# Optimization experiments

Hardware: AMD Instinct MI355X
Metric: run time of the kernel (lower is better)

The kernel has to match this reference:

```python
import jax, jax.numpy as jnp
import numpy as np

B, L, SIZE, BACK, H = 4, 1024, 1024, 512, 16
D = SIZE // H  # head_size = 64


def setup_inputs() -> dict:
    key = jax.random.key(0)
    ks = jax.random.split(key, 18)
    s = 0.02
    return {
        "k": jax.random.normal(ks[0], (B, L, SIZE), jnp.float32),
        "v": jax.random.normal(ks[1], (B, L, SIZE), jnp.float32),
        "q": jax.random.normal(ks[2], (B, L, SIZE), jnp.float32),
        "background": jax.random.normal(ks[3], (B, L, BACK), jnp.float32),
        # weights stored [in, out] (pre-transposed vs torch Linear)
        "Wk": jax.random.normal(ks[4], (SIZE, SIZE), jnp.float32) * s,
        "bk": jnp.zeros((SIZE,), jnp.float32),
        "Wv": jax.random.normal(ks[5], (SIZE, SIZE), jnp.float32) * s,
        "bv": jnp.zeros((SIZE,), jnp.float32),
        "Wq": jax.random.normal(ks[6], (SIZE, SIZE), jnp.float32) * s,
        "bq": jnp.zeros((SIZE,), jnp.float32),
        "Wb": jax.random.normal(ks[7], (BACK, SIZE), jnp.float32) * s,
        "bb": jnp.zeros((SIZE,), jnp.float32),
        "Wo": jax.random.normal(ks[8], (SIZE, SIZE), jnp.float32) * s,
        "bo": jnp.zeros((SIZE,), jnp.float32),
    }


def _heads(x):
    # [B, L, H*D] -> [B, H, L, D]
    b, l, _ = x.shape
    return x.reshape(b, l, H, D).transpose(0, 2, 1, 3)


def reference(k, v, q, background, Wk, bk, Wv, bv, Wq, bq, Wb, bb, Wo, bo):
    kh = _heads(k @ Wk + bk)
    vh = _heads(v @ Wv + bv)
    qh = _heads(q @ Wq + bq) / jnp.sqrt(jnp.asarray(D, k.dtype))
    gh = _heads(background @ Wb + bb)
    scores = jnp.einsum("bhqd,bhkd->bhqk", qh, kh)   # [B,H,Lq,Lk]
    gates = jax.nn.sigmoid(jnp.einsum("bhqd,bhkd->bhqk", qh, gh))
    attn = jax.nn.softmax(scores, axis=-1) * gates    # dropout = identity (eval)
    ctx = jnp.einsum("bhqk,bhkd->bhqd", attn, vh)
    ctx = ctx.transpose(0, 2, 1, 3).reshape(k.shape[0], -1, H * D)
    return ctx @ Wo + bo
```

## Files before the change

### kernel.cpp

```cpp
#include <hip/hip_runtime.h>
#include <cstddef>
#include <cstdint>

typedef __attribute__((ext_vector_type(8))) short s16x8;
typedef __attribute__((ext_vector_type(4))) short s16x4;
typedef __attribute__((ext_vector_type(4))) float f32x4;
typedef __attribute__((ext_vector_type(4))) unsigned u32x4;

#define MFMA(a, b, c) __builtin_amdgcn_mfma_f32_16x16x32_bf16(a, b, c, 0, 0, 0)
#define LOG2E 1.44269504088896f

__device__ __forceinline__ short f2bf(float x) {
    uint32_t u = __float_as_uint(x);
    u = (u + 0x7FFFu + ((u >> 16) & 1u)) >> 16;
    return (short)u;
}

__device__ __forceinline__ void gld16(const void* g, void* l) {
    __builtin_amdgcn_global_load_lds(
        (const __attribute__((address_space(1))) unsigned int*)g,
        (__attribute__((address_space(3))) unsigned int*)l, 16, 0, 0);
}

__device__ __forceinline__ float fexp2(float x) {
#if __has_builtin(__builtin_amdgcn_exp2f)
    return __builtin_amdgcn_exp2f(x);
#else
    return exp2f(x);
#endif
}

__device__ __forceinline__ float frcp(float x) {
#if __has_builtin(__builtin_amdgcn_rcpf)
    return __builtin_amdgcn_rcpf(x);
#else
    return 1.f / x;
#endif
}

__device__ __forceinline__ unsigned cvtpk(float lo, float hi) {
    unsigned r;
    asm("v_cvt_pk_bf16_f32 %0, %1, %2" : "=v"(r) : "v"(lo), "v"(hi));
    return r;
}

struct WtP { const float* W[5]; short* Wt[5]; int K[5]; };

__global__ __launch_bounds__(256)
void conv_wt_b(WtP p) {
    __shared__ float T[64][65];
    const int z = blockIdx.z;
    const int K = p.K[z];
    const int k0 = blockIdx.y << 6, n0 = blockIdx.x << 6;
    if (k0 >= K) return;
    const float* W = p.W[z];
    short* Wt = p.Wt[z];
    const int tr = threadIdx.x >> 4, tc4 = (threadIdx.x & 15) << 2;
    #pragma unroll
    for (int i = 0; i < 4; ++i) {
        const int r = tr + i * 16;
        const float4 v = *(const float4*)(W + (size_t)(k0 + r) * 1024 + n0 + tc4);
        T[r][tc4 + 0] = v.x; T[r][tc4 + 1] = v.y;
        T[r][tc4 + 2] = v.z; T[r][tc4 + 3] = v.w;
    }
    __syncthreads();
    #pragma unroll
    for (int i = 0; i < 4; ++i) {
        const int nr = tr + i * 16;
        s16x4 o;
        o[0] = f2bf(T[tc4 + 0][nr]); o[1] = f2bf(T[tc4 + 1][nr]);
        o[2] = f2bf(T[tc4 + 2][nr]); o[3] = f2bf(T[tc4 + 3][nr]);
        *(s16x4*)(Wt + (size_t)(n0 + nr) * K + k0 + tc4) = o;
    }
}

struct Proj5P {
    const float* Af[5];
    const short* A[5];
    const short* Bt[5]; const float* bias[5];
    void* Y[5]; int Kd[5]; float alpha[5]; int mode[5];
};

template <int F32A>
__global__ __launch_bounds__(256, 2)
void proj_gemm128d(Proj5P p, int zbase) {
    __shared__ __align__(16) short lds[2 * 16384];

    const int tid = threadIdx.x;
    const int w = tid >> 6, lane = tid & 63;
    const int la = lane & 15, kg = lane >> 4;
    const int wr = w >> 1, wc = w & 1;

    const int cpx = gridDim.x >> 3;
    const int orig = blockIdx.x;
    const int swz = (orig & 7) * cpx + (orig >> 3);
    const int z = zbase + (swz >> 8);
    const int rem = swz & 255;
    const int bm = rem >> 3, bn = rem & 7;

    const int K = p.Kd[z];
    const int NT = K >> 6;

    const int srow = tid >> 3;
    const int csrc = (tid & 7) ^ (srow & 7);
    const float* gAf = p.Af[z] ? p.Af[z] + (size_t)(bm * 128 + srow) * K + csrc * 8 : nullptr;
    const short* gA  = p.A[z]  ? p.A[z]  + (size_t)(bm * 128 + srow) * K + csrc * 8 : nullptr;
    const short* gB  = p.Bt[z] + (size_t)(bn * 128 + srow) * K + csrc * 8;
    short* dstA = &lds[srow * 64 + (tid & 7) * 8];
    short* dstB = dstA + 8192;

    float4 av[4][2];

#define STAGE_ISSUE(t, nb) do {                                            \
        const size_t ko_ = (size_t)((t) << 6);                             \
        short* bb_ = dstB + (nb) * 16384;                                  \
        _Pragma("unroll")                                                  \
        for (int i = 0; i < 4; ++i) {                                      \
            if (F32A) {                                                    \
                av[i][0] = *(const float4*)(gAf + (size_t)(32 * i) * K + ko_);     \
                av[i][1] = *(const float4*)(gAf + (size_t)(32 * i) * K + ko_ + 4); \
            } else {                                                       \
                gld16(gA + (size_t)(32 * i) * K + ko_,                     \
                      dstA + (nb) * 16384 + i * 2048);                     \
            }                                                              \
            gld16(gB + (size_t)(32 * i) * K + ko_, bb_ + i * 2048);        \
        }                                                                  \
    } while (0)

#define A_WRITE(nb) do {                                                   \
        if (F32A) {                                                        \
            _Pragma("unroll")                                              \
            for (int i = 0; i < 4; ++i) {                                  \
                u32x4 pk;                                                  \
                pk[0] = cvtpk(av[i][0].x, av[i][0].y);                     \
                pk[1] = cvtpk(av[i][0].z, av[i][0].w);                     \
                pk[2] = cvtpk(av[i][1].x, av[i][1].y);                     \
                pk[3] = cvtpk(av[i][1].z, av[i][1].w);                     \
                *(u32x4*)(dstA + (nb) * 16384 + i * 2048) = pk;            \
            }                                                              \
        }                                                                  \
    } while (0)

    const int c0 = kg ^ (la & 7), c1 = (4 + kg) ^ (la & 7);
    const int aRd = (wr * 64 + la) * 64;
    const int bRd = 8192 + (wc * 64 + la) * 64;

    f32x4 acc[4][4] = {};

    STAGE_ISSUE(0, 0);
    asm volatile("s_waitcnt vmcnt(0)" ::: "memory");
    A_WRITE(0);
    asm volatile("s_waitcnt lgkmcnt(0)" ::: "memory");
    asm volatile("s_barrier" ::: "memory");

    for (int t = 0; t < NT; ++t) {
        const int cb = (t & 1) * 16384;
        const int nb = (t & 1) ^ 1;
        if (t + 1 < NT) STAGE_ISSUE(t + 1, nb);
        s16x8 af[4][2], bf[4][2];
        #pragma unroll
        for (int m = 0; m < 4; ++m) {
            af[m][0] = *(const s16x8*)&lds[cb + aRd + m * 1024 + c0 * 8];
            af[m][1] = *(const s16x8*)&lds[cb + aRd + m * 1024 + c1 * 8];
        }
        #pragma unroll
        for (int n = 0; n < 4; ++n) {
            bf[n][0] = *(const s16x8*)&lds[cb + bRd + n * 1024 + c0 * 8];
            bf[n][1] = *(const s16x8*)&lds[cb + bRd + n * 1024 + c1 * 8];
        }
        __builtin_amdgcn_s_setprio(1);
        #pragma unroll
        for (int m = 0; m < 4; ++m)
            #pragma unroll
            for (int n = 0; n < 4; ++n) {
                acc[m][n] = MFMA(af[m][0], bf[n][0], acc[m][n]);
                acc[m][n] = MFMA(af[m][1], bf[n][1], acc[m][n]);
            }
        __builtin_amdgcn_s_setprio(0);
        if (t + 1 < NT) {
            asm volatile("s_waitcnt vmcnt(0)" ::: "memory");
            A_WRITE(nb);
            asm volatile("s_waitcnt lgkmcnt(0)" ::: "memory");
            asm volatile("s_barrier" ::: "memory");
        }
    }
#undef STAGE_ISSUE
#undef A_WRITE

    const float* __restrict__ bias = p.bias[z];
    const float alpha = p.alpha[z];
    const int mode = p.mode[z];

    if (mode == 2) {
        short* __restrict__ Y = (short*)p.Y[z];
        short* Tv = lds;
        asm volatile("s_waitcnt lgkmcnt(0)" ::: "memory");
        asm volatile("s_barrier" ::: "memory");
        #pragma unroll
        for (int ni = 0; ni < 4; ++ni) {
            const int rrow = wc * 64 + ni * 16 + la;
            const float bs = bias[bn * 128 + rrow];
            #pragma unroll
            for (int mi = 0; mi < 4; ++mi) {
                const int l0 = wr * 64 + mi * 16 + kg * 4;
                const unsigned d0 = cvtpk(alpha * (acc[mi][ni][0] + bs),
                                          alpha * (acc[mi][ni][1] + bs));
                const unsigned d1 = cvtpk(alpha * (acc[mi][ni][2] + bs),
                                          alpha * (acc[mi][ni][3] + bs));
                *(unsigned*)&Tv[rrow * 132 + l0]     = d0;
                *(unsigned*)&Tv[rrow * 132 + l0 + 2] = d1;
            }
        }
        asm volatile("s_waitcnt lgkmcnt(0)" ::: "memory");
        asm volatile("s_barrier" ::: "memory");
        const int bb_ = (bm * 128) >> 10;
        const int l0g = (bm * 128) & 1023;
        #pragma unroll
        for (int s = 0; s < 8; ++s) {
            const int c = tid + (s << 8);
            const int rr = c >> 4, seg = c & 15;
            const int hh = bn * 2 + (rr >> 6), dd = rr & 63;
            const s16x8 vv = *(const s16x8*)&Tv[rr * 132 + seg * 8];
            *(s16x8*)&Y[((((size_t)bb_ * 16 + hh) * 64 + dd) << 10) + l0g + seg * 8] = vv;
        }
        return;
    }

    #pragma unroll
    for (int n = 0; n < 4; ++n) {
        const int col = bn * 128 + wc * 64 + n * 16 + la;
        const float bs = bias[col];
        #pragma unroll
        for (int m = 0; m < 4; ++m) {
            const int row0 = bm * 128 + wr * 64 + m * 16 + kg * 4;
            #pragma unroll
            for (int r = 0; r < 4; ++r) {
                const float v = alpha * (acc[m][n][r] + bs);
                if (mode == 0) {
                    ((short*)p.Y[z])[(size_t)(row0 + r) * 1024 + col] = f2bf(v);
                } else {
                    ((float*)p.Y[z])[(size_t)(row0 + r) * 1024 + col] = v;
                }
            }
        }
    }
}

__global__ __launch_bounds__(512)
void attn_mfma(const short* __restrict__ qh, const short* __restrict__ kh,
               const short* __restrict__ gh, const short* __restrict__ vt,
               short* __restrict__ ctx) {
    __shared__ __align__(16) short lds[33792];

    const int tid = threadIdx.x, w = tid >> 6, lane = tid & 63;
    const int la = lane & 15, kg = lane >> 4;

    const int orig = blockIdx.x;
    const int xcd = orig & 7, i = orig >> 3;
    const int bh = xcd * 8 + (i >> 3);
    const int qt = i & 7;
    const int b = bh >> 4, h = bh & 15;
    const int q0 = qt << 7;

    const size_t hb = ((size_t)b << 20) + ((size_t)h << 6);
    const size_t vtbase = ((size_t)bh) << 16;

    const int qrow = q0 + w * 16 + la;
    const s16x8 aq0 = *(const s16x8*)(qh + hb + (size_t)qrow * 1024 + kg * 8);
    const s16x8 aq1 = *(const s16x8*)(qh + hb + (size_t)qrow * 1024 + 32 + kg * 8);

    const int sr = tid >> 3, sc = tid & 7;
    const int cs = sc ^ (sr & 7);
    const short* ksrc = kh + hb + (size_t)sr * 1024 + cs * 8;
    const short* gsrc = gh + hb + (size_t)sr * 1024 + cs * 8;
    const short* vsrc = vt + vtbase + (size_t)sr * 1024 + cs * 8;
    const int sdst = tid * 8;

    const int ch0 = (kg ^ (la & 7)) * 8;
    const int ch1 = ((4 + kg) ^ (la & 7)) * 8;
    const int pbase = 24576 + w * 1152;

    float s_run = 0.f;
    f32x4 o[4] = {};

#define ASTG(kt, bb) do {                                                  \
        const size_t kr_ = (size_t)((kt) << 6) * 1024;                     \
        gld16(ksrc + kr_, &lds[(bb) * 4096 + sdst]);                       \
        gld16(gsrc + kr_, &lds[8192 + (bb) * 4096 + sdst]);                \
        gld16(vsrc + ((kt) << 6), &lds[16384 + (bb) * 4096 + sdst]);       \
    } while (0)

    ASTG(0, 0);
    asm volatile("s_waitcnt vmcnt(0)" ::: "memory");
    asm volatile("s_barrier" ::: "memory");

    for (int kt = 0; kt < 16; ++kt) {
        const int cb = (kt & 1) * 4096;
        if (kt < 15) ASTG(kt + 1, (kt + 1) & 1);

        f32x4 st[4] = {}, gt[4] = {};
        #pragma unroll
        for (int nf = 0; nf < 4; ++nf) {
            const int rb = cb + (nf * 16 + la) * 64;
            const s16x8 kb0 = *(const s16x8*)&lds[rb + ch0];
            const s16x8 kb1 = *(const s16x8*)&lds[rb + ch1];
            st[nf] = MFMA(kb0, aq0, st[nf]);
            st[nf] = MFMA(kb1, aq1, st[nf]);
            const s16x8 gb0 = *(const s16x8*)&lds[8192 + rb + ch0];
            const s16x8 gb1 = *(const s16x8*)&lds[8192 + rb + ch1];
            gt[nf] = MFMA(gb0, aq0, gt[nf]);
            gt[nf] = MFMA(gb1, aq1, gt[nf]);
        }

        float ps = 0.f;
        unsigned pkw[4][2];
        #pragma unroll
        for (int nf = 0; nf < 4; ++nf) {
            const float p0 = fexp2(st[nf][0]);
            const float p1 = fexp2(st[nf][1]);
            const float p2 = fexp2(st[nf][2]);
            const float p3 = fexp2(st[nf][3]);
            ps += (p0 + p1) + (p2 + p3);
            const float g0 = frcp(1.f + fexp2(-gt[nf][0]));
            const float g1 = frcp(1.f + fexp2(-gt[nf][1]));
            const float g2 = frcp(1.f + fexp2(-gt[nf][2]));
            const float g3 = frcp(1.f + fexp2(-gt[nf][3]));
            pkw[nf][0] = cvtpk(p0 * g0, p1 * g1);
            pkw[nf][1] = cvtpk(p2 * g2, p3 * g3);
        }
        s_run += ps;

        #pragma unroll
        for (int nf = 0; nf < 4; ++nf) {
            *(unsigned*)&lds[pbase + la * 72 + nf * 16 + kg * 4]     = pkw[nf][0];
            *(unsigned*)&lds[pbase + la * 72 + nf * 16 + kg * 4 + 2] = pkw[nf][1];
        }

        const s16x8 pa0 = *(const s16x8*)&lds[pbase + la * 72 + kg * 8];
        const s16x8 pa1 = *(const s16x8*)&lds[pbase + la * 72 + 32 + kg * 8];
        #pragma unroll
        for (int nf = 0; nf < 4; ++nf) {
            const int rb = cb + (nf * 16 + la) * 64;
            const s16x8 vb0 = *(const s16x8*)&lds[16384 + rb + ch0];
            const s16x8 vb1 = *(const s16x8*)&lds[16384 + rb + ch1];
            o[nf] = MFMA(vb0, pa0, o[nf]);
            o[nf] = MFMA(vb1, pa1, o[nf]);
        }

        if (kt < 15) {
            asm volatile("s_waitcnt vmcnt(0)" ::: "memory");
            asm volatile("s_barrier" ::: "memory");
        }
    }
#undef ASTG

    float sv = s_run;
    sv += __shfl_xor(sv, 16);
    sv += __shfl_xor(sv, 32);
    const float inv = frcp(sv);
    short* crow = ctx + ((size_t)(b * 1024 + qrow) << 10) + (h << 6);
    #pragma unroll
    for (int nf = 0; nf < 4; ++nf) {
        *(unsigned*)(crow + nf * 16 + kg * 4)     = cvtpk(o[nf][0] * inv, o[nf][1] * inv);
        *(unsigned*)(crow + nf * 16 + kg * 4 + 2) = cvtpk(o[nf][2] * inv, o[nf][3] * inv);
    }
}

extern "C" void kernel_launch(void* const* d_in, const int* in_sizes, int n_in,
                              void* d_out, int out_size, void* d_ws, size_t ws_size,
                              hipStream_t stream) {
    (void)in_sizes; (void)n_in; (void)out_size; (void)ws_size;

    const float* k  = (const float*)d_in[0];
    const float* v  = (const float*)d_in[1];
    const float* q  = (const float*)d_in[2];
    const float* bg = (const float*)d_in[3];
    const float* Wk = (const float*)d_in[4];  const float* bk = (const float*)d_in[5];
    const float* Wv = (const float*)d_in[6];  const float* bv = (const float*)d_in[7];
    const float* Wq = (const float*)d_in[8];  const float* bq = (const float*)d_in[9];
    const float* Wb = (const float*)d_in[10]; const float* bb = (const float*)d_in[11];
    const float* Wo = (const float*)d_in[12]; const float* bo = (const float*)d_in[13];

    short* ws = (short*)d_ws;
    const size_t MN = (size_t)4096 * 1024;
    short* khb  = ws;
    short* qhb  = ws + MN;
    short* ghb  = ws + 2 * MN;
    short* vtb  = ws + 3 * MN;
    short* ctxb = ws + 4 * MN;
    short* wkt  = ws + 5 * MN;
    short* wvt  = wkt + 1048576;
    short* wqt  = wvt + 1048576;
    short* wot  = wqt + 1048576;
    short* wbt  = wot + 1048576;

    const dim3 blk(256);

    WtP wp;
    wp.W[0] = Wk; wp.Wt[0] = wkt; wp.K[0] = 1024;
    wp.W[1] = Wv; wp.Wt[1] = wvt; wp.K[1] = 1024;
    wp.W[2] = Wq; wp.Wt[2] = wqt; wp.K[2] = 1024;
    wp.W[3] = Wb; wp.Wt[3] = wbt; wp.K[3] = 512;
    wp.W[4] = Wo; wp.Wt[4] = wot; wp.K[4] = 1024;
    conv_wt_b<<<dim3(16, 16, 5), blk, 0, stream>>>(wp);

    Proj5P p5;
    p5.Af[0] = k;  p5.A[0] = nullptr; p5.Bt[0] = wkt; p5.bias[0] = bk;
    p5.Y[0] = khb; p5.Kd[0] = 1024; p5.alpha[0] = LOG2E;  p5.mode[0] = 0;
    p5.Af[1] = q;  p5.A[1] = nullptr; p5.Bt[1] = wqt; p5.bias[1] = bq;
    p5.Y[1] = qhb; p5.Kd[1] = 1024; p5.alpha[1] = 0.125f; p5.mode[1] = 0;
    p5.Af[2] = bg; p5.A[2] = nullptr; p5.Bt[2] = wbt; p5.bias[2] = bb;
    p5.Y[2] = ghb; p5.Kd[2] = 512;  p5.alpha[2] = LOG2E;  p5.mode[2] = 0;
    p5.Af[3] = v;  p5.A[3] = nullptr; p5.Bt[3] = wvt; p5.bias[3] = bv;
    p5.Y[3] = vtb; p5.Kd[3] = 1024; p5.alpha[3] = 1.0f;   p5.mode[3] = 2;
    p5.Af[4] = nullptr; p5.A[4] = ctxb; p5.Bt[4] = wot; p5.bias[4] = bo;
    p5.Y[4] = d_out; p5.Kd[4] = 1024; p5.alpha[4] = 1.0f; p5.mode[4] = 1;

    proj_gemm128d<1><<<dim3(1024), blk, 0, stream>>>(p5, 0);
    attn_mfma<<<dim3(512), dim3(512), 0, stream>>>(qhb, khb, ghb, vtb, ctxb);
    proj_gemm128d<0><<<dim3(256), blk, 0, stream>>>(p5, 4);
}
```

Measured before the change: 116.0 us.

## Deepen fp32 A prefetch in projection GEMM and add narrow-tile output GEMM

```diff
diff --git a/kernel.cpp b/kernel.cpp
--- a/kernel.cpp
+++ b/kernel.cpp
@@ -81,9 +81,8 @@
     void* Y[5]; int Kd[5]; float alpha[5]; int mode[5];
 };
 
-template <int F32A>
 __global__ __launch_bounds__(256, 2)
-void proj_gemm128d(Proj5P p, int zbase) {
+void proj_gemm128f(Proj5P p) {
     __shared__ __align__(16) short lds[2 * 16384];
 
     const int tid = threadIdx.x;
@@ -91,10 +90,9 @@
     const int la = lane & 15, kg = lane >> 4;
     const int wr = w >> 1, wc = w & 1;
 
-    const int cpx = gridDim.x >> 3;
     const int orig = blockIdx.x;
-    const int swz = (orig & 7) * cpx + (orig >> 3);
-    const int z = zbase + (swz >> 8);
+    const int swz = (orig & 7) * 128 + (orig >> 3);
+    const int z = swz >> 8;
     const int rem = swz & 255;
     const int bm = rem >> 3, bn = rem & 7;
 
@@ -103,41 +101,37 @@
 
     const int srow = tid >> 3;
     const int csrc = (tid & 7) ^ (srow & 7);
-    const float* gAf = p.Af[z] ? p.Af[z] + (size_t)(bm * 128 + srow) * K + csrc * 8 : nullptr;
-    const short* gA  = p.A[z]  ? p.A[z]  + (size_t)(bm * 128 + srow) * K + csrc * 8 : nullptr;
+    const float* gAf = p.Af[z] + (size_t)(bm * 128 + srow) * K + csrc * 8;
     const short* gB  = p.Bt[z] + (size_t)(bn * 128 + srow) * K + csrc * 8;
     short* dstA = &lds[srow * 64 + (tid & 7) * 8];
     short* dstB = dstA + 8192;
 
     float4 av[4][2];
 
-#define STAGE_ISSUE(t, nb) do {                                            \
+#define ISSUE_A(t) do {                                                    \
         const size_t ko_ = (size_t)((t) << 6);                             \
-        short* bb_ = dstB + (nb) * 16384;                                  \
         _Pragma("unroll")                                                  \
         for (int i = 0; i < 4; ++i) {                                      \
-            if (F32A) {                                                    \
-                av[i][0] = *(const float4*)(gAf + (size_t)(32 * i) * K + ko_);     \
-                av[i][1] = *(const float4*)(gAf + (size_t)(32 * i) * K + ko_ + 4); \
-            } else {                                                       \
-                gld16(gA + (size_t)(32 * i) * K + ko_,                     \
-                      dstA + (nb) * 16384 + i * 2048);                     \
-            }                                                              \
-            gld16(gB + (size_t)(32 * i) * K + ko_, bb_ + i * 2048);        \
+            av[i][0] = *(const float4*)(gAf + (size_t)(32 * i) * K + ko_);     \
+            av[i][1] = *(const float4*)(gAf + (size_t)(32 * i) * K + ko_ + 4); \
         }                                                                  \
     } while (0)
-
+#define ISSUE_B(t, nb) do {                                                \
+        const size_t ko_ = (size_t)((t) << 6);                             \
+        _Pragma("unroll")                                                  \
+        for (int i = 0; i < 4; ++i)                                        \
+            gld16(gB + (size_t)(32 * i) * K + ko_,                         \
+                  dstB + (nb) * 16384 + i * 2048);                         \
+    } while (0)
 #define A_WRITE(nb) do {                                                   \
-        if (F32A) {                                                        \
-            _Pragma("unroll")                                              \
-            for (int i = 0; i < 4; ++i) {                                  \
-                u32x4 pk;                                                  \
-                pk[0] = cvtpk(av[i][0].x, av[i][0].y);                     \
-                pk[1] = cvtpk(av[i][0].z, av[i][0].w);                     \
-                pk[2] = cvtpk(av[i][1].x, av[i][1].y);                     \
-                pk[3] = cvtpk(av[i][1].z, av[i][1].w);                     \
-                *(u32x4*)(dstA + (nb) * 16384 + i * 2048) = pk;            \
-            }                                                              \
+        _Pragma("unroll")                                                  \
+        for (int i = 0; i < 4; ++i) {                                      \
+            u32x4 pk;                                                      \
+            pk[0] = cvtpk(av[i][0].x, av[i][0].y);                         \
+            pk[1] = cvtpk(av[i][0].z, av[i][0].w);                         \
+            pk[2] = cvtpk(av[i][1].x, av[i][1].y);                         \
+            pk[3] = cvtpk(av[i][1].z, av[i][1].w);                         \
+            *(u32x4*)(dstA + (nb) * 16384 + i * 2048) = pk;                \
         }                                                                  \
     } while (0)
 
@@ -147,16 +141,17 @@
 
     f32x4 acc[4][4] = {};
 
-    STAGE_ISSUE(0, 0);
-    asm volatile("s_waitcnt vmcnt(0)" ::: "memory");
+    ISSUE_A(0);
+    ISSUE_B(0, 0);
     A_WRITE(0);
-    asm volatile("s_waitcnt lgkmcnt(0)" ::: "memory");
+    asm volatile("s_waitcnt vmcnt(0) lgkmcnt(0)" ::: "memory");
     asm volatile("s_barrier" ::: "memory");
+    ISSUE_A(1);
 
     for (int t = 0; t < NT; ++t) {
         const int cb = (t & 1) * 16384;
-        const int nb = (t & 1) ^ 1;
-        if (t + 1 < NT) STAGE_ISSUE(t + 1, nb);
+        const int nbi = (t & 1) ^ 1;
+        if (t + 1 < NT) ISSUE_B(t + 1, nbi);
         s16x8 af[4][2], bf[4][2];
         #pragma unroll
         for (int m = 0; m < 4; ++m) {
@@ -178,13 +173,19 @@
             }
         __builtin_amdgcn_s_setprio(0);
         if (t + 1 < NT) {
-            asm volatile("s_waitcnt vmcnt(0)" ::: "memory");
-            A_WRITE(nb);
+            A_WRITE(nbi);
+            if (t + 2 < NT) {
+                ISSUE_A(t + 2);
+                asm volatile("s_waitcnt vmcnt(8)" ::: "memory");
+            } else {
+                asm volatile("s_waitcnt vmcnt(0)" ::: "memory");
+            }
             asm volatile("s_waitcnt lgkmcnt(0)" ::: "memory");
             asm volatile("s_barrier" ::: "memory");
         }
     }
-#undef STAGE_ISSUE
+#undef ISSUE_A
+#undef ISSUE_B
 #undef A_WRITE
 
     const float* __restrict__ bias = p.bias[z];
@@ -236,12 +237,98 @@
             #pragma unroll
             for (int r = 0; r < 4; ++r) {
                 const float v = alpha * (acc[m][n][r] + bs);
-                if (mode == 0) {
-                    ((short*)p.Y[z])[(size_t)(row0 + r) * 1024 + col] = f2bf(v);
-                } else {
-                    ((float*)p.Y[z])[(size_t)(row0 + r) * 1024 + col] = v;
-                }
+                ((short*)p.Y[z])[(size_t)(row0 + r) * 1024 + col] = f2bf(v);
             }
+        }
+    }
+}
+
+__global__ __launch_bounds__(256, 3)
+void proj_gemmO(Proj5P p) {
+    __shared__ __align__(16) short lds[2 * 12288];
+
+    const int tid = threadIdx.x;
+    const int w = tid >> 6, lane = tid & 63;
+    const int la = lane & 15, kg = lane >> 4;
+    const int wr = w >> 1, wc = w & 1;
+
+    const int orig = blockIdx.x;
+    const int swz = (orig & 7) * 64 + (orig >> 3);
+    const int bm = swz >> 4, bn = swz & 15;
+
+    const int K = 1024, NT = 16;
+
+    const int srow = tid >> 3;
+    const int csrc = (tid & 7) ^ (srow & 7);
+    const short* gA = p.A[4]  + (size_t)(bm * 128 + srow) * K + csrc * 8;
+    const short* gB = p.Bt[4] + (size_t)(bn * 64 + srow) * K + csrc * 8;
+    short* dstA = &lds[srow * 64 + (tid & 7) * 8];
+    short* dstB = dstA + 8192;
+
+#define STAGE(t, nb) do {                                                  \
+        const size_t ko_ = (size_t)((t) << 6);                             \
+        _Pragma("unroll")                                                  \
+        for (int i = 0; i < 4; ++i)                                        \
+            gld16(gA + (size_t)(32 * i) * K + ko_,                         \
+                  dstA + (nb) * 12288 + i * 2048);                         \
+        _Pragma("unroll")                                                  \
+        for (int i = 0; i < 2; ++i)                                        \
+            gld16(gB + (size_t)(32 * i) * K + ko_,                         \
+                  dstB + (nb) * 12288 + i * 2048);                         \
+    } while (0)
+
+    const int c0 = kg ^ (la & 7), c1 = (4 + kg) ^ (la & 7);
+    const int aRd = (wr * 64 + la) * 64;
+    const int bRd = 8192 + (wc * 32 + la) * 64;
+
+    f32x4 acc[4][2] = {};
+
+    STAGE(0, 0);
+    asm volatile("s_waitcnt vmcnt(0)" ::: "memory");
+    asm volatile("s_barrier" ::: "memory");
+
+    for (int t = 0; t < NT; ++t) {
+        const int cb = (t & 1) * 12288;
+        if (t + 1 < NT) STAGE(t + 1, (t & 1) ^ 1);
+        s16x8 af[4][2], bf[2][2];
+        #pragma unroll
+        for (int m = 0; m < 4; ++m) {
+            af[m][0] = *(const s16x8*)&lds[cb + aRd + m * 1024 + c0 * 8];
+            af[m][1] = *(const s16x8*)&lds[cb + aRd + m * 1024 + c1 * 8];
+        }
+        #pragma unroll
+        for (int n = 0; n < 2; ++n) {
+            bf[n][0] = *(const s16x8*)&lds[cb + bRd + n * 1024 + c0 * 8];
+            bf[n][1] = *(const s16x8*)&lds[cb + bRd + n * 1024 + c1 * 8];
+        }
+        __builtin_amdgcn_s_setprio(1);
+        #pragma unroll
+        for (int m = 0; m < 4; ++m)
+            #pragma unroll
+            for (int n = 0; n < 2; ++n) {
+                acc[m][n] = MFMA(af[m][0], bf[n][0], acc[m][n]);
+                acc[m][n] = MFMA(af[m][1], bf[n][1], acc[m][n]);
+            }
+        __builtin_amdgcn_s_setprio(0);
+        if (t + 1 < NT) {
+            asm volatile("s_waitcnt vmcnt(0)" ::: "memory");
+            asm volatile("s_barrier" ::: "memory");
+        }
+    }
+#undef STAGE
+
+    const float* __restrict__ bias = p.bias[4];
+    float* __restrict__ Y = (float*)p.Y[4];
+    #pragma unroll
+    for (int n = 0; n < 2; ++n) {
+        const int col = bn * 64 + wc * 32 + n * 16 + la;
+        const float bs = bias[col];
+        #pragma unroll
+        for (int m = 0; m < 4; ++m) {
+            const int row0 = bm * 128 + wr * 64 + m * 16 + kg * 4;
+            #pragma unroll
+            for (int r = 0; r < 4; ++r)
+                Y[(size_t)(row0 + r) * 1024 + col] = acc[m][n][r] + bs;
         }
     }
 }
@@ -416,7 +503,7 @@
     p5.Af[4] = nullptr; p5.A[4] = ctxb; p5.Bt[4] = wot; p5.bias[4] = bo;
     p5.Y[4] = d_out; p5.Kd[4] = 1024; p5.alpha[4] = 1.0f; p5.mode[4] = 1;
 
-    proj_gemm128d<1><<<dim3(1024), blk, 0, stream>>>(p5, 0);
+    proj_gemm128f<<<dim3(1024), blk, 0, stream>>>(p5);
     attn_mfma<<<dim3(512), dim3(512), 0, stream>>>(qhb, khb, ghb, vtb, ctxb);
-    proj_gemm128d<0><<<dim3(256), blk, 0, stream>>>(p5, 4);
-}
+    proj_gemmO<<<dim3(512), blk, 0, stream>>>(p5);
+}
```

Result: faster. 106.6 us, median of 3 (-8.1%).
